# Optimization experiments

Hardware: AMD Instinct MI355X
Metric: run time of the kernel (lower is better)

Reference implementation:

```python
import jax, jax.numpy as jnp
import numpy as np

N_NODES = 100000
N_EDGES = 1600000
N_GRAPHS = 128


def _gcn_norm(edge_index, n_nodes):
    # Add self-loops, then symmetric normalization deg^-1/2 * A_hat * deg^-1/2 (PyG GCNConv default).
    loops = jnp.arange(n_nodes, dtype=edge_index.dtype)
    src = jnp.concatenate([edge_index[0], loops])
    dst = jnp.concatenate([edge_index[1], loops])
    deg = jax.ops.segment_sum(jnp.ones_like(src, dtype=jnp.float32), dst, num_segments=n_nodes)
    dinv = jnp.where(deg > 0, jax.lax.rsqrt(deg), 0.0)
    norm = dinv[src] * dinv[dst]  # [E + N]
    return src, dst, norm


def _gcn_conv(x, W, b, src, dst, norm, n_nodes):
    h = x @ W                      # [N, out] linear transform first (small GEMM)
    msg = h[src] * norm[:, None]   # gather + per-edge scale
    out = jax.ops.segment_sum(msg, dst, num_segments=n_nodes)  # scatter-add
    return out + b


def setup_inputs() -> dict:
    key = jax.random.key(0)
    ks = jax.random.split(key, 6)
    x = jax.random.normal(ks[0], (N_NODES, 3), dtype=jnp.float32)
    edge_index = jax.random.randint(ks[1], (2, N_EDGES), 0, N_NODES, dtype=jnp.int64)
    batch = jnp.sort(jax.random.randint(ks[2], (N_NODES,), 0, N_GRAPHS, dtype=jnp.int64))
    W1 = jax.random.normal(ks[3], (3, 64), dtype=jnp.float32) * (1.0 / np.sqrt(3.0))
    b1 = jnp.zeros((64,), dtype=jnp.float32)
    W2 = jax.random.normal(ks[4], (64, 128), dtype=jnp.float32) * (1.0 / np.sqrt(64.0))
    b2 = jnp.zeros((128,), dtype=jnp.float32)
    return {"x": x, "edge_index": edge_index, "batch": batch,
            "W1": W1, "b1": b1, "W2": W2, "b2": b2}


def reference(x, edge_index, batch, W1, b1, W2, b2):
    n_nodes = x.shape[0]
    src, dst, norm = _gcn_norm(edge_index, n_nodes)
    h = jax.nn.relu(_gcn_conv(x, W1, b1, src, dst, norm, n_nodes))
    h = _gcn_conv(h, W2, b2, src, dst, norm, n_nodes)
    # global mean pool over graphs in the batch
    sums = jax.ops.segment_sum(h, batch, num_segments=N_GRAPHS)
    counts = jax.ops.segment_sum(jnp.ones((n_nodes,), dtype=h.dtype), batch, num_segments=N_GRAPHS)
    return sums / jnp.maximum(counts, 1.0)[:, None]
```

## Files before the change

kernel.cpp:

```cpp
#include <hip/hip_runtime.h>
#include <hip/hip_bf16.h>


typedef __hip_bfloat16 bf16;
#define NGRAPH 128
#define NSLICE 8
#define TILE_S 4096
#define CAPLG  13
#define SCAP   8192

__device__ __forceinline__ float b2f(bf16 v) { return __bfloat162float(v); }
__device__ __forceinline__ float fld(const void* p, long long i, int isbf) {
    return isbf ? b2f(((const bf16*)p)[i]) : ((const float*)p)[i];
}
__device__ __forceinline__ int ild(const void* p, long long i, int is64) {
    return is64 ? (int)((const long long*)p)[i] : ((const int*)p)[i];
}
__device__ __forceinline__ unsigned short f2bf(float f) {
    bf16 h = __float2bfloat16(f);
    return *reinterpret_cast<unsigned short*>(&h);
}
__device__ __forceinline__ int probe_is64(const void* ei) {
    int lane = threadIdx.x & 63;
    const int* w = (const int*)ei;
    unsigned long long bz = __ballot(w[2 * lane + 1] == 0);
    return (__popcll(bz) >= 56) ? 1 : 0;
}
__device__ __forceinline__ int probe_isbf(const void* x) {
    int lane = threadIdx.x & 63;
    const unsigned short* u = (const unsigned short*)x;
    int e0 = (u[2 * lane] >> 7) & 0xFF;
    int e1 = (u[2 * (lane + 64)] >> 7) & 0xFF;
    int good = __popcll(__ballot(e0 >= 90 && e0 <= 135))
             + __popcll(__ballot(e1 >= 90 && e1 <= 135));
    return (good >= 96) ? 1 : 0;
}
__device__ __forceinline__ int wave_iscan(int v, int lane) {
#pragma unroll
    for (int d = 1; d < 64; d <<= 1) {
        int t = __shfl_up(v, d);
        if (lane >= d) v += t;
    }
    return v;
}

__global__ void k_split(const void* __restrict__ ei, unsigned* __restrict__ edges2,
                        int* __restrict__ gcur, float4* __restrict__ P4,
                        int E, int NB) {
    for (int k = blockIdx.x * 512 + threadIdx.x; k < NSLICE * NGRAPH * 16;
         k += gridDim.x * 512)
        P4[k] = make_float4(0.f, 0.f, 0.f, 0.f);
    __shared__ int hist[512], scan_[512], gbase[512], lcur[512];
    __shared__ int2 stage[TILE_S];
    int i = threadIdx.x;
    int lane = i & 63, wv = i >> 6;
    int is64 = probe_is64(ei);
    long long base = (long long)blockIdx.x * TILE_S;
    int lim = (int)min((long long)TILE_S, (long long)E - base);
    hist[i] = 0;
    __syncthreads();
    int dreg[8], sreg[8];
    if (lim == TILE_S && (E & 7) == 0) {
        long long e0 = base + ((long long)i << 3);
        if (is64) {
            const int4* pd = (const int4*)((const long long*)ei + E + e0);
            const int4* ps = (const int4*)((const long long*)ei + e0);
#pragma unroll
            for (int j = 0; j < 4; ++j) {
                int4 d4 = pd[j]; int4 s4 = ps[j];
                dreg[2 * j] = d4.x; dreg[2 * j + 1] = d4.z;
                sreg[2 * j] = s4.x; sreg[2 * j + 1] = s4.z;
            }
        } else {
            const int4* pd = (const int4*)((const int*)ei + E + e0);
            const int4* ps = (const int4*)((const int*)ei + e0);
#pragma unroll
            for (int j = 0; j < 2; ++j) {
                int4 d4 = pd[j]; int4 s4 = ps[j];
                dreg[4 * j] = d4.x; dreg[4 * j + 1] = d4.y;
                dreg[4 * j + 2] = d4.z; dreg[4 * j + 3] = d4.w;
                sreg[4 * j] = s4.x; sreg[4 * j + 1] = s4.y;
                sreg[4 * j + 2] = s4.z; sreg[4 * j + 3] = s4.w;
            }
        }
#pragma unroll
        for (int j = 0; j < 8; ++j) atomicAdd(&hist[dreg[j] >> 8], 1);
    } else {
#pragma unroll
        for (int j = 0; j < 8; ++j) {
            int k = i + (j << 9);
            if (k < lim) {
                dreg[j] = ild(ei, (long long)E + base + k, is64);
                sreg[j] = ild(ei, base + k, is64);
                atomicAdd(&hist[dreg[j] >> 8], 1);
            } else dreg[j] = -1;
        }
    }
    __syncthreads();
    int v = hist[i];
    int isc = wave_iscan(v, lane);
    if (lane == 63) gbase[wv] = isc;
    __syncthreads();
    int sbase = 0;
    for (int s = 0; s < wv; ++s) sbase += gbase[s];
    scan_[i] = sbase + isc - v;
    __syncthreads();
    if (i < NB) {
        lcur[i] = scan_[i];
        gbase[i] = hist[i] ? atomicAdd(&gcur[i], hist[i]) : 0;
    }
    __syncthreads();
#pragma unroll
    for (int j = 0; j < 8; ++j) {
        if (dreg[j] >= 0) {
            int p = atomicAdd(&lcur[dreg[j] >> 8], 1);
            stage[p] = make_int2(dreg[j], sreg[j]);
        }
    }
    __syncthreads();
    for (int t = i; t < lim; t += 512) {
        int2 r = stage[t];
        int b = r.x >> 8;
        edges2[((size_t)b << CAPLG) + gbase[b] + (t - scan_[b])] =
            (unsigned)r.y | ((unsigned)(r.x & 255) << 24);
    }
}

__global__ void k_deg(const unsigned* __restrict__ edges2, const int* __restrict__ gcur,
                      const void* __restrict__ batch, const void* __restrict__ x,
                      const void* __restrict__ ei,
                      float4* __restrict__ xs, int* __restrict__ deg,
                      int* __restrict__ start, int N) {
    __shared__ int hist[256];
    int b = blockIdx.x;
    int node0 = b << 8;
    int nloc = min(256, N - node0);
    int is64 = probe_is64(ei);
    int isbf = probe_isbf(x);
    int i = threadIdx.x;
    if (i < 256) hist[i] = 0;
    __syncthreads();
    size_t rbase = (size_t)b << CAPLG;
    int rcnt = gcur[b];
    for (int t4 = i << 2; t4 < rcnt; t4 += 2048) {
        uint4 r4 = *(const uint4*)(edges2 + rbase + t4);
        atomicAdd(&hist[r4.x >> 24], 1);
        if (t4 + 1 < rcnt) atomicAdd(&hist[r4.y >> 24], 1);
        if (t4 + 2 < rcnt) atomicAdd(&hist[r4.z >> 24], 1);
        if (t4 + 3 < rcnt) atomicAdd(&hist[r4.w >> 24], 1);
    }
    __syncthreads();
    if (i < nloc) {
        int node = node0 + i;
        int dg = hist[i];
        deg[node] = dg;
        float di = rsqrtf((float)(dg + 1));
        xs[node] = make_float4(di * fld(x, 3LL * node, isbf),
                               di * fld(x, 3LL * node + 1, isbf),
                               di * fld(x, 3LL * node + 2, isbf), 0.0f);
        int g = ild(batch, node, is64);
        int gp = (node == 0) ? -1 : ild(batch, node - 1, is64);
        for (int q = gp + 1; q <= g; ++q) start[q] = node;
        if (node == N - 1)
            for (int q = g + 1; q <= NGRAPH; ++q) start[q] = N;
    }
}

__global__ void k_sortl1(const unsigned* __restrict__ edges2, const void* __restrict__ batch,
                         const void* __restrict__ x, const void* __restrict__ ei,
                         const int* __restrict__ gcur,
                         const int* __restrict__ deg, const float4* __restrict__ xs,
                         const void* __restrict__ W1, const void* __restrict__ b1,
                         unsigned* __restrict__ meta, bf16* __restrict__ hs1, int N) {
    __shared__ int loff[257], lcur[256], sc[256];
    __shared__ unsigned gdeg[256];
    __shared__ unsigned stage[SCAP];
    __shared__ float w[256];
    __shared__ float ag[256][4];
    int b = blockIdx.x;
    int node0 = b << 8;
    int nloc = min(256, N - node0);
    int is64 = probe_is64(ei);
    int isbf = probe_isbf(x);
    int i = threadIdx.x;
    int lane = i & 63, wv = i >> 6;
    if (i < 192) w[i] = fld(W1, i, isbf);
    if (i >= 192 && i < 256) w[i] = fld(b1, i - 192, isbf);
    size_t rbase = (size_t)b << CAPLG;
    int rcnt = gcur[b];
    int partial = 0;
    for (int j = i; j < b; j += 512) partial += gcur[j];
#pragma unroll
    for (int d = 1; d < 64; d <<= 1) partial += __shfl_xor(partial, d);
    if (lane == 0) sc[wv] = partial;
    __syncthreads();
    int mbase = sc[0] + sc[1] + sc[2] + sc[3] + sc[4] + sc[5] + sc[6] + sc[7] + node0;
    __syncthreads();
    unsigned rc[8];
    {
        int t8 = i << 3;
        uint4 a = *(const uint4*)(edges2 + rbase + t8);
        uint4 c = *(const uint4*)(edges2 + rbase + t8 + 4);
        rc[0] = a.x; rc[1] = a.y; rc[2] = a.z; rc[3] = a.w;
        rc[4] = c.x; rc[5] = c.y; rc[6] = c.z; rc[7] = c.w;
        int ncache = min(rcnt, 4096);
#pragma unroll
        for (int j = 0; j < 8; ++j)
            if (t8 + j >= ncache) rc[j] = 0xFFFFFFFFu;
    }
    int dg = (i < nloc) ? deg[node0 + i] : 0;
    int v = (i < nloc) ? dg + 1 : 0;
    int isc = 0;
    if (i < 256) isc = wave_iscan(v, lane);
    if (i < 256 && lane == 63) sc[wv] = isc;
    __syncthreads();
    if (i < 256) {
        int sbase = 0;
        for (int s = 0; s < wv; ++s) sbase += sc[s];
        if (i < nloc) loff[i] = sbase + isc - v;
        if (i == nloc - 1) loff[nloc] = sbase + isc;
    }
    __syncthreads();
    if (i < nloc) {
        int node = node0 + i;
        int g = ild(batch, node, is64);
        unsigned gd = ((unsigned)g << 17) | ((unsigned)min(dg, 255) << 24);
        gdeg[i] = gd;
        lcur[i] = loff[i] + 1;
        stage[loff[i]] = (unsigned)node | gd;
    }
    __syncthreads();
#pragma unroll
    for (int j = 0; j < 8; ++j) {
        if (rc[j] != 0xFFFFFFFFu) {
            int dl = (int)(rc[j] >> 24);
            int p = atomicAdd(&lcur[dl], 1);
            if (p < SCAP) stage[p] = (rc[j] & 0x1FFFFu) | gdeg[dl];
        }
    }
    for (int t = 4096 + i; t < rcnt; t += 512) {
        unsigned r = edges2[rbase + t];
        int dl = (int)(r >> 24);
        int p = atomicAdd(&lcur[dl], 1);
        if (p < SCAP) stage[p] = (r & 0x1FFFFu) | gdeg[dl];
    }
    __syncthreads();
    int total = loff[nloc];
    int totc = min(total, SCAP);
    {
        int head = (4 - (mbase & 3)) & 3;
        if (head > totc) head = totc;
        if (i < head) meta[mbase + i] = stage[i];
        int nvec = (totc - head) >> 2;
        for (int c = i; c < nvec; c += 512) {
            int t = head + (c << 2);
            *(uint4*)(meta + mbase + t) =
                make_uint4(stage[t], stage[t + 1], stage[t + 2], stage[t + 3]);
        }
        for (int t = head + (nvec << 2) + i; t < totc; t += 512)
            meta[mbase + t] = stage[t];
    }
    if (i < nloc) {
        float ax = 0.f, ay = 0.f, az = 0.f;
        int p1 = min(loff[i + 1], SCAP);
        for (int p = loff[i]; p < p1; ++p) {
            float4 vv = xs[stage[p] & 0x1FFFFu];
            ax += vv.x; ay += vv.y; az += vv.z;
        }
        float di = rsqrtf((float)(dg + 1));
        ag[i][0] = di * ax; ag[i][1] = di * ay; ag[i][2] = di * az;
        ag[i][3] = di;
    }
    __syncthreads();
    for (int t = i << 2; t < (nloc << 6); t += 2048) {
        int ii = t >> 6, j = t & 63;
        float a0 = ag[ii][0], a1 = ag[ii][1], a2 = ag[ii][2], di = ag[ii][3];
        ushort4 o;
        o.x = f2bf(di * fmaxf(a0 * w[j] + a1 * w[64 + j] + a2 * w[128 + j] + w[192 + j], 0.f));
        o.y = f2bf(di * fmaxf(a0 * w[j + 1] + a1 * w[65 + j] + a2 * w[129 + j] + w[193 + j], 0.f));
        o.z = f2bf(di * fmaxf(a0 * w[j + 2] + a1 * w[66 + j] + a2 * w[130 + j] + w[194 + j], 0.f));
        o.w = f2bf(di * fmaxf(a0 * w[j + 3] + a1 * w[67 + j] + a2 * w[131 + j] + w[195 + j], 0.f));
        *(ushort4*)(hs1 + (size_t)(node0 + ii) * 64 + j) = o;
    }
}

__global__ void k_gather2(const uint4* __restrict__ hs1q, const unsigned* __restrict__ meta,
                          float* __restrict__ P, int Etot, int chunk) {
    int wid = (blockIdx.x * blockDim.x + threadIdx.x) >> 6;
    int lane = threadIdx.x & 63;
    int q = lane >> 3;
    int l8 = lane & 7;
    long long base = (long long)wid * chunk;
    if (base >= Etot) return;
    long long end = base + chunk;
    if (end > Etot) end = Etot;
    float acc[8] = {0.f, 0.f, 0.f, 0.f, 0.f, 0.f, 0.f, 0.f};
    int gcur = -1;
#define GFLUSH()                                                                \
    if (gcur >= 0) {                                                            \
        float* dp = P + (size_t)q * (NGRAPH * 64) + (size_t)gcur * 64 + (l8 << 3); \
        _Pragma("unroll")                                                       \
        for (int k = 0; k < 8; ++k) { atomicAdd(dp + k, acc[k]); acc[k] = 0.f; }\
    }
#define STEP(m, v)                                                              \
    {                                                                           \
        int g = (int)((m >> 17) & 0x7Fu);                                       \
        float w = rsqrtf((float)((m >> 24) & 0xFFu) + 1.0f);                    \
        if (g != gcur) { GFLUSH(); gcur = g; }                                  \
        acc[0] += w * __uint_as_float(v.x << 16);                               \
        acc[1] += w * __uint_as_float(v.x & 0xFFFF0000u);                       \
        acc[2] += w * __uint_as_float(v.y << 16);                               \
        acc[3] += w * __uint_as_float(v.y & 0xFFFF0000u);                       \
        acc[4] += w * __uint_as_float(v.z << 16);                               \
        acc[5] += w * __uint_as_float(v.z & 0xFFFF0000u);                       \
        acc[6] += w * __uint_as_float(v.w << 16);                               \
        acc[7] += w * __uint_as_float(v.w & 0xFFFF0000u);                       \
    }
    long long p = base + q;
    for (; p + 24 < end; p += 32) {
        unsigned m0 = meta[p];
        unsigned m1 = meta[p + 8];
        unsigned m2 = meta[p + 16];
        unsigned m3 = meta[p + 24];
        uint4 v0 = hs1q[(size_t)(m0 & 0x1FFFFu) * 8 + l8];
        uint4 v1 = hs1q[(size_t)(m1 & 0x1FFFFu) * 8 + l8];
        uint4 v2 = hs1q[(size_t)(m2 & 0x1FFFFu) * 8 + l8];
        uint4 v3 = hs1q[(size_t)(m3 & 0x1FFFFu) * 8 + l8];
        STEP(m0, v0) STEP(m1, v1) STEP(m2, v2) STEP(m3, v3)
    }
    for (; p < end; p += 8) {
        unsigned m = meta[p];
        uint4 v = hs1q[(size_t)(m & 0x1FFFFu) * 8 + l8];
        STEP(m, v)
    }
    {
        int g0 = __shfl(gcur, 0);
        if (g0 >= 0 && __all(gcur == g0)) {
#pragma unroll
            for (int k = 0; k < 8; ++k) {
                acc[k] += __shfl_xor(acc[k], 8);
                acc[k] += __shfl_xor(acc[k], 16);
                acc[k] += __shfl_xor(acc[k], 32);
            }
            if (q == 0) {
                float* dp = P + (size_t)(wid & (NSLICE - 1)) * (NGRAPH * 64)
                              + (size_t)g0 * 64 + (l8 << 3);
#pragma unroll
                for (int k = 0; k < 8; ++k) atomicAdd(dp + k, acc[k]);
            }
        } else {
            GFLUSH();
        }
    }
#undef STEP
#undef GFLUSH
}

__global__ void k_out(const float* __restrict__ P, const int* __restrict__ start,
                      const void* __restrict__ W2, const void* __restrict__ b2v,
                      const void* __restrict__ x, void* __restrict__ out) {
    __shared__ float pm[64];
    int isbf = probe_isbf(x);
    int g = blockIdx.x, j = threadIdx.x;
    int c = start[g + 1] - start[g];
    if (j < 64) {
        float v = 0.f;
        for (int s = 0; s < NSLICE; ++s) v += P[(size_t)s * NGRAPH * 64 + g * 64 + j];
        pm[j] = (c > 0) ? v / (float)c : 0.0f;
    }
    __syncthreads();
    float acc = 0.0f;
    if (c > 0) {
        acc = fld(b2v, j, isbf);
        for (int k = 0; k < 64; ++k) acc += pm[k] * fld(W2, k * 128 + j, isbf);
    }
    if (isbf) ((bf16*)out)[g * 128 + j] = __float2bfloat16(acc);
    else      ((float*)out)[g * 128 + j] = acc;
}

extern "C" void kernel_launch(void* const* d_in, const int* in_sizes, int n_in,
                              void* d_out, int out_size, void* d_ws, size_t ws_size,
                              hipStream_t stream) {
    const void* x    = d_in[0];
    const void* ei   = d_in[1];
    const void* batch= d_in[2];
    const void* W1   = d_in[3];
    const void* b1   = d_in[4];
    const void* W2   = d_in[5];
    const void* b2   = d_in[6];

    const int N = in_sizes[0] / 3;
    const int E = in_sizes[1] / 2;
    const int Etot = E + N;
    const int NB = (N + 255) / 256;

    char* ws = (char*)d_ws;
    size_t off = 0;
    auto alloc = [&](size_t bytes) {
        size_t o = off;
        off = (off + bytes + 511) & ~(size_t)511;
        return o;
    };
    int* gcur     = (int*)(ws + alloc((size_t)NB * 4));
    int* start    = (int*)(ws + alloc((size_t)(NGRAPH + 1) * 4));
    int* deg      = (int*)(ws + alloc((size_t)N * 4));
    unsigned* edges2 = (unsigned*)(ws + alloc(((size_t)NB << CAPLG) * 4));
    unsigned* meta= (unsigned*)(ws + alloc((size_t)Etot * 4 + 64));
    float4* xs    = (float4*)(ws + alloc((size_t)N * 16));
    bf16* hs1     = (bf16*)(ws + alloc((size_t)N * 64 * 2));
    float* P      = (float*)(ws + alloc((size_t)NSLICE * NGRAPH * 64 * 4));
    (void)ws_size;

    (void)hipMemsetAsync(gcur, 0, (size_t)NB * 4, stream);

    const int sb = (E + TILE_S - 1) / TILE_S;

    const int g2blocks = 2048;
    const int g2waves = g2blocks * 4;
    const int chunk = (Etot + g2waves - 1) / g2waves;

    k_split<<<sb, 512, 0, stream>>>(ei, edges2, gcur, (float4*)P, E, NB);
    k_deg<<<NB, 512, 0, stream>>>(edges2, gcur, batch, x, ei, xs, deg, start, N);
    k_sortl1<<<NB, 512, 0, stream>>>(edges2, batch, x, ei, gcur, deg, xs,
                                     W1, b1, meta, hs1, N);
    k_gather2<<<g2blocks, 256, 0, stream>>>((const uint4*)hs1, meta, P, Etot, chunk);
    k_out<<<NGRAPH, 128, 0, stream>>>(P, start, W2, b2, x, d_out);
}
```

Measured before the change: 174.6 us.

## Halve split tile size and split sort/layer-1 kernel into two half-bucket blocks

The edge-split kernel now processes 2048 edges per block instead of 4096, which doubles its block count and cuts the register and shared staging each block needs. The sort/layer-1 kernel launches two blocks per 256-node bucket. Each block handles 128 destination nodes, with a smaller shared stage buffer and correspondingly offset meta and hs1 writes. This aims to raise occupancy and parallelism for these kernels, at the cost of each half-block rereading the whole bucket's edges and redoing the bucket-wide prefix scan.

```diff
diff --git a/kernel.cpp b/kernel.cpp
--- a/kernel.cpp
+++ b/kernel.cpp
@@ -5,9 +5,9 @@
 typedef __hip_bfloat16 bf16;
 #define NGRAPH 128
 #define NSLICE 8
-#define TILE_S 4096
+#define TILE_S 2048
 #define CAPLG  13
-#define SCAP   8192
+#define HSCAP  4608
 
 __device__ __forceinline__ float b2f(bf16 v) { return __bfloat162float(v); }
 __device__ __forceinline__ float fld(const void* p, long long i, int isbf) {
@@ -59,35 +59,29 @@
     int lim = (int)min((long long)TILE_S, (long long)E - base);
     hist[i] = 0;
     __syncthreads();
-    int dreg[8], sreg[8];
-    if (lim == TILE_S && (E & 7) == 0) {
-        long long e0 = base + ((long long)i << 3);
+    int dreg[4], sreg[4];
+    if (lim == TILE_S && (E & 3) == 0) {
+        long long e0 = base + ((long long)i << 2);
         if (is64) {
             const int4* pd = (const int4*)((const long long*)ei + E + e0);
             const int4* ps = (const int4*)((const long long*)ei + e0);
 #pragma unroll
-            for (int j = 0; j < 4; ++j) {
+            for (int j = 0; j < 2; ++j) {
                 int4 d4 = pd[j]; int4 s4 = ps[j];
                 dreg[2 * j] = d4.x; dreg[2 * j + 1] = d4.z;
                 sreg[2 * j] = s4.x; sreg[2 * j + 1] = s4.z;
             }
         } else {
-            const int4* pd = (const int4*)((const int*)ei + E + e0);
-            const int4* ps = (const int4*)((const int*)ei + e0);
-#pragma unroll
-            for (int j = 0; j < 2; ++j) {
-                int4 d4 = pd[j]; int4 s4 = ps[j];
-                dreg[4 * j] = d4.x; dreg[4 * j + 1] = d4.y;
-                dreg[4 * j + 2] = d4.z; dreg[4 * j + 3] = d4.w;
-                sreg[4 * j] = s4.x; sreg[4 * j + 1] = s4.y;
-                sreg[4 * j + 2] = s4.z; sreg[4 * j + 3] = s4.w;
-            }
-        }
-#pragma unroll
-        for (int j = 0; j < 8; ++j) atomicAdd(&hist[dreg[j] >> 8], 1);
+            int4 d4 = *(const int4*)((const int*)ei + E + e0);
+            int4 s4 = *(const int4*)((const int*)ei + e0);
+            dreg[0] = d4.x; dreg[1] = d4.y; dreg[2] = d4.z; dreg[3] = d4.w;
+            sreg[0] = s4.x; sreg[1] = s4.y; sreg[2] = s4.z; sreg[3] = s4.w;
+        }
+#pragma unroll
+        for (int j = 0; j < 4; ++j) atomicAdd(&hist[dreg[j] >> 8], 1);
     } else {
 #pragma unroll
-        for (int j = 0; j < 8; ++j) {
+        for (int j = 0; j < 4; ++j) {
             int k = i + (j << 9);
             if (k < lim) {
                 dreg[j] = ild(ei, (long long)E + base + k, is64);
@@ -111,7 +105,7 @@
     }
     __syncthreads();
 #pragma unroll
-    for (int j = 0; j < 8; ++j) {
+    for (int j = 0; j < 4; ++j) {
         if (dreg[j] >= 0) {
             int p = atomicAdd(&lcur[dreg[j] >> 8], 1);
             stage[p] = make_int2(dreg[j], sreg[j]);
@@ -172,14 +166,19 @@
                          const int* __restrict__ deg, const float4* __restrict__ xs,
                          const void* __restrict__ W1, const void* __restrict__ b1,
                          unsigned* __restrict__ meta, bf16* __restrict__ hs1, int N) {
-    __shared__ int loff[257], lcur[256], sc[256];
-    __shared__ unsigned gdeg[256];
-    __shared__ unsigned stage[SCAP];
+    __shared__ int loff[257], lcur[128], sc[256];
+    __shared__ unsigned gdeg[128];
+    __shared__ unsigned stage[HSCAP];
     __shared__ float w[256];
-    __shared__ float ag[256][4];
-    int b = blockIdx.x;
+    __shared__ float ag[128][4];
+    int bb = blockIdx.x;
+    int b = bb >> 1, h = bb & 1;
     int node0 = b << 8;
     int nloc = min(256, N - node0);
+    int lo = h << 7;
+    if (lo >= nloc) return;
+    int hi = min(nloc, lo + 128);
+    int nr = hi - lo;
     int is64 = probe_is64(ei);
     int isbf = probe_isbf(x);
     int i = threadIdx.x;
@@ -208,8 +207,7 @@
         for (int j = 0; j < 8; ++j)
             if (t8 + j >= ncache) rc[j] = 0xFFFFFFFFu;
     }
-    int dg = (i < nloc) ? deg[node0 + i] : 0;
-    int v = (i < nloc) ? dg + 1 : 0;
+    int v = (i < nloc) ? deg[node0 + i] + 1 : 0;
     int isc = 0;
     if (i < 256) isc = wave_iscan(v, lane);
     if (i < 256 && lane == 63) sc[wv] = isc;
@@ -221,58 +219,67 @@
         if (i == nloc - 1) loff[nloc] = sbase + isc;
     }
     __syncthreads();
-    if (i < nloc) {
+    int loff0 = loff[lo];
+    if (i >= lo && i < hi) {
+        int il = i - lo;
         int node = node0 + i;
+        int dg = v - 1;
         int g = ild(batch, node, is64);
         unsigned gd = ((unsigned)g << 17) | ((unsigned)min(dg, 255) << 24);
-        gdeg[i] = gd;
-        lcur[i] = loff[i] + 1;
-        stage[loff[i]] = (unsigned)node | gd;
+        gdeg[il] = gd;
+        int p0 = loff[i] - loff0;
+        lcur[il] = p0 + 1;
+        if (p0 < HSCAP) stage[p0] = (unsigned)node | gd;
     }
     __syncthreads();
 #pragma unroll
     for (int j = 0; j < 8; ++j) {
         if (rc[j] != 0xFFFFFFFFu) {
             int dl = (int)(rc[j] >> 24);
-            int p = atomicAdd(&lcur[dl], 1);
-            if (p < SCAP) stage[p] = (rc[j] & 0x1FFFFu) | gdeg[dl];
+            if (dl >= lo && dl < hi) {
+                int p = atomicAdd(&lcur[dl - lo], 1);
+                if (p < HSCAP) stage[p] = (rc[j] & 0x1FFFFu) | gdeg[dl - lo];
+            }
         }
     }
     for (int t = 4096 + i; t < rcnt; t += 512) {
         unsigned r = edges2[rbase + t];
         int dl = (int)(r >> 24);
-        int p = atomicAdd(&lcur[dl], 1);
-        if (p < SCAP) stage[p] = (r & 0x1FFFFu) | gdeg[dl];
-    }
-    __syncthreads();
-    int total = loff[nloc];
-    int totc = min(total, SCAP);
+        if (dl >= lo && dl < hi) {
+            int p = atomicAdd(&lcur[dl - lo], 1);
+            if (p < HSCAP) stage[p] = (r & 0x1FFFFu) | gdeg[dl - lo];
+        }
+    }
+    __syncthreads();
+    int totc = min(loff[hi] - loff0, HSCAP);
+    int mb = mbase + loff0;
     {
-        int head = (4 - (mbase & 3)) & 3;
+        int head = (4 - (mb & 3)) & 3;
         if (head > totc) head = totc;
-        if (i < head) meta[mbase + i] = stage[i];
+        if (i < head) meta[mb + i] = stage[i];
         int nvec = (totc - head) >> 2;
         for (int c = i; c < nvec; c += 512) {
             int t = head + (c << 2);
-            *(uint4*)(meta + mbase + t) =
+            *(uint4*)(meta + mb + t) =
                 make_uint4(stage[t], stage[t + 1], stage[t + 2], stage[t + 3]);
         }
         for (int t = head + (nvec << 2) + i; t < totc; t += 512)
-            meta[mbase + t] = stage[t];
-    }
-    if (i < nloc) {
+            meta[mb + t] = stage[t];
+    }
+    if (i < nr) {
         float ax = 0.f, ay = 0.f, az = 0.f;
-        int p1 = min(loff[i + 1], SCAP);
-        for (int p = loff[i]; p < p1; ++p) {
+        int p0 = loff[lo + i] - loff0;
+        int p1 = min(loff[lo + i + 1] - loff0, HSCAP);
+        for (int p = p0; p < p1; ++p) {
             float4 vv = xs[stage[p] & 0x1FFFFu];
             ax += vv.x; ay += vv.y; az += vv.z;
         }
-        float di = rsqrtf((float)(dg + 1));
+        float di = rsqrtf((float)(deg[node0 + lo + i] + 1));
         ag[i][0] = di * ax; ag[i][1] = di * ay; ag[i][2] = di * az;
         ag[i][3] = di;
     }
     __syncthreads();
-    for (int t = i << 2; t < (nloc << 6); t += 2048) {
+    for (int t = i << 2; t < (nr << 6); t += 2048) {
         int ii = t >> 6, j = t & 63;
         float a0 = ag[ii][0], a1 = ag[ii][1], a2 = ag[ii][2], di = ag[ii][3];
         ushort4 o;
@@ -280,7 +287,7 @@
         o.y = f2bf(di * fmaxf(a0 * w[j + 1] + a1 * w[65 + j] + a2 * w[129 + j] + w[193 + j], 0.f));
         o.z = f2bf(di * fmaxf(a0 * w[j + 2] + a1 * w[66 + j] + a2 * w[130 + j] + w[194 + j], 0.f));
         o.w = f2bf(di * fmaxf(a0 * w[j + 3] + a1 * w[67 + j] + a2 * w[131 + j] + w[195 + j], 0.f));
-        *(ushort4*)(hs1 + (size_t)(node0 + ii) * 64 + j) = o;
+        *(ushort4*)(hs1 + (size_t)(node0 + lo + ii) * 64 + j) = o;
     }
 }
 
@@ -421,8 +428,8 @@
 
     k_split<<<sb, 512, 0, stream>>>(ei, edges2, gcur, (float4*)P, E, NB);
     k_deg<<<NB, 512, 0, stream>>>(edges2, gcur, batch, x, ei, xs, deg, start, N);
-    k_sortl1<<<NB, 512, 0, stream>>>(edges2, batch, x, ei, gcur, deg, xs,
-                                     W1, b1, meta, hs1, N);
+    k_sortl1<<<2 * NB, 512, 0, stream>>>(edges2, batch, x, ei, gcur, deg, xs,
+                                         W1, b1, meta, hs1, N);
     k_gather2<<<g2blocks, 256, 0, stream>>>((const uint4*)hs1, meta, P, Etot, chunk);
     k_out<<<NGRAPH, 128, 0, stream>>>(P, start, W2, b2, x, d_out);
 }
```

Result: no change. 177.5 us (+1.7%).
